# Optimization experiments

Measured on AMD Instinct MI355X. Metric: run time of the kernel, lower is better.

## Reference

```python
import jax, jax.numpy as jnp
import numpy as np

LN_EPS = 1e-12


def _conv1d(x, w, b, pad):
    # x: (B, Cin, L), w: (Cout, Cin, K) -> (B, Cout, L)
    y = jax.lax.conv_general_dilated(x, w, window_strides=(1,), padding=[(pad, pad)],
                                     dimension_numbers=('NCH', 'OIH', 'NCH'))
    return y + b[None, :, None]


def setup_inputs() -> dict:
    key = jax.random.key(0)
    ks = jax.random.split(key, 6)
    B, L, C, KH = 4, 4096, 768, 7
    return {
        'hidden_states': jax.random.normal(ks[0], (B, L, C), jnp.float32),
        'attention_mask': jnp.ones((B, L), jnp.float32),
        'special_tokens_mask': jnp.zeros((B, L), jnp.float32),
        'ln_w': jnp.ones((C,), jnp.float32),
        'ln_b': jnp.zeros((C,), jnp.float32),
        'off_w': jax.random.normal(ks[1], (KH, C, KH), jnp.float32) * 0.02,
        'off_b': jnp.zeros((KH,), jnp.float32),
        'mod_w': jax.random.normal(ks[2], (KH, C, KH), jnp.float32) * 0.02,
        'mod_b': jnp.zeros((KH,), jnp.float32),
        'reg_w': jax.random.normal(ks[3], (C, C, KH), jnp.float32) * 0.02,
    }


def reference(hidden_states, attention_mask, special_tokens_mask,
              ln_w, ln_b, off_w, off_b, mod_w, mod_b, reg_w):
    B, L, C = hidden_states.shape
    kh = off_w.shape[0]
    pad = kh // 2
    residual = hidden_states

    # input layernorm (biased variance, like torch.nn.LayerNorm)
    mu = hidden_states.mean(-1, keepdims=True)
    var = hidden_states.var(-1, keepdims=True)
    h = (hidden_states - mu) * jax.lax.rsqrt(var + LN_EPS) * ln_w + ln_b

    ht = jnp.swapaxes(h, 1, 2)  # (B, C, L)
    off = _conv1d(ht, off_w, off_b, pad)                    # (B, kh, L) seq-axis offsets
    mod = 2.0 * jax.nn.sigmoid(_conv1d(ht, mod_w, mod_b, pad))  # (B, kh, L)

    # mask special tokens / padding before sampling
    gate = ((1.0 - special_tokens_mask) * attention_mask)[:, None, :]
    xm = ht * gate  # (B, C, L)

    # deformable 1D sampling positions: p - pad + k + off[b,k,p]
    base = (jnp.arange(L, dtype=jnp.float32) - pad)[None, :] + jnp.arange(kh, dtype=jnp.float32)[:, None]  # (kh, L)
    pos = base[None, :, :] + off  # (B, kh, L)
    f = jnp.floor(pos)
    t = pos - f                   # (B, kh, L) frac
    fi = f.astype(jnp.int32)

    def gather(idx):
        # linear-sample tap with zero padding outside [0, L-1]
        inb = ((idx >= 0) & (idx <= L - 1)).astype(xm.dtype)  # (B, kh, L)
        idxc = jnp.clip(idx, 0, L - 1)
        v = jax.vmap(lambda xb, ib: xb[:, ib])(xm, idxc)      # (B, C, kh, L)
        return v * inb[:, None, :, :]

    sample = gather(fi) * (1.0 - t)[:, None] + gather(fi + 1) * t[:, None]  # (B, C, kh, L)
    sample = sample * mod[:, None]  # modulated

    out = jnp.einsum('ock,bckp->bop', reg_w, sample)  # (B, C, L)
    out = jnp.swapaxes(out, 1, 2) + residual          # (B, L, C)
    return out
```

## Files before the change

kernel.cpp:

```cpp
#include <hip/hip_runtime.h>
#include <math.h>

#define BB 4
#define LL 4096
#define CC 768
#define KHH 7
#define PADK 3
#define ROWS (BB*LL)
#define NKP  (BB*KHH*LL)
#define GK   (KHH*CC)
#define NT   (GK/64)
#define NKC  (GK/8)

typedef unsigned short ushort8 __attribute__((ext_vector_type(8)));
typedef unsigned short ushort4v __attribute__((ext_vector_type(4)));
typedef short short8 __attribute__((ext_vector_type(8)));
typedef float f32x4 __attribute__((ext_vector_type(4)));
typedef unsigned int uint4v __attribute__((ext_vector_type(4)));

__device__ __forceinline__ float bf2f(unsigned short u) {
    return __uint_as_float(((unsigned)u) << 16);
}
__device__ __forceinline__ unsigned short f2bf(float x) {
    unsigned u = __float_as_uint(x);
    return (unsigned short)((u + 0x7FFFu + ((u >> 16) & 1u)) >> 16);
}
__device__ __forceinline__ unsigned cvtpk(float lo, float hi) {
    unsigned r;
    asm("v_cvt_pk_bf16_f32 %0, %1, %2" : "=v"(r) : "v"(lo), "v"(hi));
    return r;
}

__global__ __launch_bounds__(64) void k_ln(const float* __restrict__ x,
        const float* __restrict__ mask, const float* __restrict__ special,
        const float* __restrict__ lnw, const float* __restrict__ lnb,
        unsigned short* __restrict__ hb, float* __restrict__ gate) {
    int row = blockIdx.x;
    int t = threadIdx.x;
    const float4* xr = (const float4*)(x + (size_t)row * CC);
    float4 v0 = xr[t], v1 = xr[t + 64], v2 = xr[t + 128];
    float s = v0.x + v0.y + v0.z + v0.w
            + v1.x + v1.y + v1.z + v1.w
            + v2.x + v2.y + v2.z + v2.w;
    float q = v0.x * v0.x + v0.y * v0.y + v0.z * v0.z + v0.w * v0.w
            + v1.x * v1.x + v1.y * v1.y + v1.z * v1.z + v1.w * v1.w
            + v2.x * v2.x + v2.y * v2.y + v2.z * v2.z + v2.w * v2.w;
    for (int o = 32; o; o >>= 1) { s += __shfl_xor(s, o); q += __shfl_xor(q, o); }
    float mu  = s * (1.f / CC);
    float var = fmaxf(q * (1.f / CC) - mu * mu, 0.f);
    float rstd = rsqrtf(var + 1e-12f);
    const float4* lw = (const float4*)lnw;
    const float4* lb = (const float4*)lnb;
    ushort4v* hr = (ushort4v*)(hb + (size_t)row * CC);
#pragma unroll
    for (int j = 0; j < 3; ++j) {
        int i4 = t + 64 * j;
        float4 v = (j == 0) ? v0 : (j == 1) ? v1 : v2;
        float4 w = lw[i4], bso = lb[i4];
        ushort4v r;
        r[0] = f2bf((v.x - mu) * rstd * w.x + bso.x);
        r[1] = f2bf((v.y - mu) * rstd * w.y + bso.y);
        r[2] = f2bf((v.z - mu) * rstd * w.z + bso.z);
        r[3] = f2bf((v.w - mu) * rstd * w.w + bso.w);
        hr[i4] = r;
    }
    if (t == 0) gate[row] = (1.f - special[row]) * mask[row];
}

__global__ __launch_bounds__(256) void k_wbt(const float* __restrict__ rw,
                                             unsigned short* __restrict__ wbt) {
    __shared__ float s[4 * GK];
    int o0 = blockIdx.x * 4;
    for (int i = threadIdx.x; i < 4 * GK; i += 256)
        s[i] = rw[(size_t)(o0 + i / GK) * GK + (i % GK)];
    __syncthreads();
    for (int kc = threadIdx.x; kc < NKC; kc += 256) {
        int k = kc / 96;
        int c0 = (kc - k * 96) * 8;
        unsigned short* dst = wbt + ((size_t)kc * CC + o0) * 8;
#pragma unroll
        for (int oo = 0; oo < 4; ++oo) {
            ushort8 r;
#pragma unroll
            for (int e = 0; e < 8; ++e) r[e] = f2bf(s[oo * GK + (c0 + e) * KHH + k]);
            *(ushort8*)(dst + oo * 8) = r;
        }
    }
}

__global__ __launch_bounds__(256) void k_wcb(const float* __restrict__ ow, const float* __restrict__ mw,
                                             unsigned short* __restrict__ wcb) {
    int i = blockIdx.x;
    for (int c = threadIdx.x; c < CC; c += 256) {
        float v = 0.f;
        if (i < 49)      v = ow[(size_t)(i / 7) * (CC * KHH) + (size_t)c * KHH + (i % 7)];
        else if (i < 98) { int j = i - 49; v = mw[(size_t)(j / 7) * (CC * KHH) + (size_t)c * KHH + (j % 7)]; }
        wcb[(size_t)i * CC + c] = f2bf(v);
    }
}

__global__ __launch_bounds__(256) void k_dg2(const unsigned short* __restrict__ A,
        const unsigned short* __restrict__ Bm, float* __restrict__ d) {
    __shared__ __align__(16) char As[64 * 128];
    __shared__ __align__(16) char Bs[128 * 128];
    int r0 = blockIdx.x * 64;
    int t = threadIdx.x;
    int lane = t & 63, w = t >> 6;
    int wr = w >> 1, wc = w & 1;
    f32x4 acc[2][4];
#pragma unroll
    for (int m = 0; m < 2; ++m)
#pragma unroll
        for (int n = 0; n < 4; ++n) acc[m][n] = (f32x4){0.f, 0.f, 0.f, 0.f};
    int lr = lane & 15;
    int lkb0 = (lane >> 4) * 16;
    for (int kk = 0; kk < CC; kk += 64) {
#pragma unroll
        for (int s = 0; s < 2; ++s) {
            int byteoff = (s * 256 + t) * 16;
            int row = byteoff >> 7;
            int colb = byteoff & 127;
            int sw = (row * 128 + colb) ^ ((row & 7) << 4);
            *(ushort8*)(As + sw) = *(const ushort8*)(A + (size_t)(r0 + row) * CC + kk + (colb >> 1));
        }
#pragma unroll
        for (int s = 0; s < 4; ++s) {
            int byteoff = (s * 256 + t) * 16;
            int row = byteoff >> 7;
            int colb = byteoff & 127;
            int sw = (row * 128 + colb) ^ ((row & 7) << 4);
            *(ushort8*)(Bs + sw) = *(const ushort8*)(Bm + (size_t)row * CC + kk + (colb >> 1));
        }
        __syncthreads();
#pragma unroll
        for (int ks = 0; ks < 2; ++ks) {
            short8 av[2], bv[4];
            int lkb = lkb0 + ks * 64;
#pragma unroll
            for (int m = 0; m < 2; ++m) {
                int ar = wr * 32 + m * 16 + lr;
                av[m] = *(const short8*)(As + ((ar * 128 + lkb) ^ ((ar & 7) << 4)));
            }
#pragma unroll
            for (int n = 0; n < 4; ++n) {
                int br = wc * 64 + n * 16 + lr;
                bv[n] = *(const short8*)(Bs + ((br * 128 + lkb) ^ ((br & 7) << 4)));
            }
#pragma unroll
            for (int m = 0; m < 2; ++m)
#pragma unroll
                for (int n = 0; n < 4; ++n)
                    acc[m][n] = __builtin_amdgcn_mfma_f32_16x16x32_bf16(av[m], bv[n], acc[m][n], 0, 0, 0);
        }
        __syncthreads();
    }
    int lr4 = (lane >> 4) * 4, lc = lane & 15;
#pragma unroll
    for (int m = 0; m < 2; ++m) {
        int gr = r0 + wr * 32 + m * 16 + lr4;
#pragma unroll
        for (int n = 0; n < 4; ++n) {
            int gc = wc * 64 + n * 16 + lc;
#pragma unroll
            for (int j = 0; j < 4; ++j)
                d[(size_t)(gr + j) * 128 + gc] = acc[m][n][j];
        }
    }
}

__global__ __launch_bounds__(256) void k_off(const float* __restrict__ d,
        const float* __restrict__ offb, const float* __restrict__ modb,
        const float* __restrict__ gate,
        int* __restrict__ idx0, int* __restrict__ idx1,
        float* __restrict__ w0a, float* __restrict__ w1a) {
    int flat = blockIdx.x * 256 + threadIdx.x;
    if (flat >= NKP) return;
    int p = flat & (LL - 1);
    int k = (flat >> 12) % KHH;
    int b = flat / (KHH * LL);
    float offa = offb[k], moda = modb[k];
#pragma unroll
    for (int j = 0; j < KHH; ++j) {
        int q = p + j - PADK;
        if (q >= 0 && q < LL) {
            const float* dr = d + (size_t)(b * LL + q) * 128;
            offa += dr[k * 7 + j];
            moda += dr[49 + k * 7 + j];
        }
    }
    float modv = 2.f / (1.f + expf(-moda));
    float pos = (float)(p - PADK + k) + offa;
    pos = fminf(fmaxf(pos, -1.0e9f), 1.0e9f);
    float f = floorf(pos);
    float tf = pos - f;
    int i0 = (int)f;
    int i1 = i0 + 1;
    float in0 = (i0 >= 0 && i0 < LL) ? 1.f : 0.f;
    float in1 = (i1 >= 0 && i1 < LL) ? 1.f : 0.f;
    int c0 = min(max(i0, 0), LL - 1);
    int c1 = min(max(i1, 0), LL - 1);
    float g0 = gate[b * LL + c0] * in0;
    float g1 = gate[b * LL + c1] * in1;
    w0a[flat] = modv * (1.f - tf) * g0;
    w1a[flat] = modv * tf * g1;
    idx0[flat] = c0;
    idx1[flat] = c1;
}


#define STEPOFF 49152
#define KSOFF   24576

#define LOADB3(Q, KS, D0, D1, D2) do { \
    const unsigned short* _q = (Q) + (KS) * KSOFF; \
    D0 = *(const short8*)(_q); \
    D1 = *(const short8*)(_q + 128); \
    D2 = *(const short8*)(_q + 256); \
} while (0)

#define MFMA_ROW3(AV, M, B0, B1, B2) \
    acc[M][0] = __builtin_amdgcn_mfma_f32_16x16x32_bf16(AV, B0, acc[M][0], 0, 0, 0); \
    acc[M][1] = __builtin_amdgcn_mfma_f32_16x16x32_bf16(AV, B1, acc[M][1], 0, 0, 0); \
    acc[M][2] = __builtin_amdgcn_mfma_f32_16x16x32_bf16(AV, B2, acc[M][2], 0, 0, 0);

#define COMPUTE_KS3(ASB, KS, B0, B1, B2) do { \
    __builtin_amdgcn_s_setprio(1); \
    int _lkb = ke0 * 2 + (KS) * 64; \
    short8 _av0, _av1, _av2, _av3, _av4, _av5, _av6, _av7; \
    { int ar = 0 * 16 + lr; _av0 = *(const short8*)((ASB) + ar * 128 + (_lkb ^ ((ar & 7) << 4))); } \
    { int ar = 1 * 16 + lr; _av1 = *(const short8*)((ASB) + ar * 128 + (_lkb ^ ((ar & 7) << 4))); } \
    { int ar = 2 * 16 + lr; _av2 = *(const short8*)((ASB) + ar * 128 + (_lkb ^ ((ar & 7) << 4))); } \
    { int ar = 3 * 16 + lr; _av3 = *(const short8*)((ASB) + ar * 128 + (_lkb ^ ((ar & 7) << 4))); } \
    MFMA_ROW3(_av0, 0, B0, B1, B2) \
    MFMA_ROW3(_av1, 1, B0, B1, B2) \
    MFMA_ROW3(_av2, 2, B0, B1, B2) \
    MFMA_ROW3(_av3, 3, B0, B1, B2) \
    { int ar = 4 * 16 + lr; _av4 = *(const short8*)((ASB) + ar * 128 + (_lkb ^ ((ar & 7) << 4))); } \
    { int ar = 5 * 16 + lr; _av5 = *(const short8*)((ASB) + ar * 128 + (_lkb ^ ((ar & 7) << 4))); } \
    { int ar = 6 * 16 + lr; _av6 = *(const short8*)((ASB) + ar * 128 + (_lkb ^ ((ar & 7) << 4))); } \
    { int ar = 7 * 16 + lr; _av7 = *(const short8*)((ASB) + ar * 128 + (_lkb ^ ((ar & 7) << 4))); } \
    MFMA_ROW3(_av4, 4, B0, B1, B2) \
    MFMA_ROW3(_av5, 5, B0, B1, B2) \
    MFMA_ROW3(_av6, 6, B0, B1, B2) \
    MFMA_ROW3(_av7, 7, B0, B1, B2) \
    __builtin_amdgcn_s_setprio(0); \
} while (0)

#define BAR() do { \
    asm volatile("s_waitcnt lgkmcnt(0)" ::: "memory"); \
    __builtin_amdgcn_s_barrier(); \
    __builtin_amdgcn_sched_barrier(0); \
} while (0)

__global__ __launch_bounds__(512, 2) void k_fgemm(const unsigned short* __restrict__ hb,
        const unsigned short* __restrict__ Wbt,
        const int* __restrict__ idx0, const int* __restrict__ idx1,
        const float* __restrict__ w0a, const float* __restrict__ w1a,
        const float* __restrict__ resid, float* __restrict__ out) {
    __shared__ __align__(16) char As[2][128 * 128];

    int bid = blockIdx.x;
    int nhalf = (bid & 7) >> 2;
    int rowtile = (bid >> 3) * 4 + (bid & 3);
    int r0 = rowtile * 128;
    int o0 = nhalf * 384;
    int b = r0 >> 12;
    int p0 = r0 & (LL - 1);
    int pbase = ((b * KHH) << 12) + p0;
    const unsigned short* hbB = hb + (size_t)b * LL * CC;

    int t = threadIdx.x;
    int lane = t & 63, wc = t >> 6;
    int lr = lane & 15;
    int ke0 = (lane >> 4) * 8;

    const unsigned short* pB = Wbt + ((size_t)(lane >> 4) * CC + o0 + wc * 48 + lr) * 8;

    int arow = t >> 2, aseg = t & 3;
    int acolb = aseg * 32;
    int aswz0 = arow * 128 + (acolb ^ ((arow & 7) << 4));
    int aswz1 = arow * 128 + ((acolb + 16) ^ ((arow & 7) << 4));

    f32x4 acc[8][3];
#pragma unroll
    for (int m = 0; m < 8; ++m)
#pragma unroll
        for (int n = 0; n < 3; ++n) acc[m][n] = (f32x4){0.f, 0.f, 0.f, 0.f};

    float wa = 0.f, wbv = 0.f;
    int cur_tap = -1;
    const unsigned short* pA0 = hbB;
    const unsigned short* pA1 = hbB;

    ushort8 la0, la1, la2, la3;
    short8 S0_0, S0_1, S0_2;
    short8 S1_0, S1_1, S1_2;
    short8 S2_0, S2_1, S2_2;

    auto loadA = [&](int tap, int c0) {
        if (tap != cur_tap) {
            int pf = pbase + (tap << 12) + arow;
            int g0 = idx0[pf], g1 = idx1[pf];
            wa = w0a[pf];  wbv = w1a[pf];
            cur_tap = tap;
            pA0 = hbB + (size_t)g0 * CC + c0 + aseg * 16;
            pA1 = hbB + (size_t)g1 * CC + c0 + aseg * 16;
        } else {
            pA0 += 64;
            pA1 += 64;
        }
        la0 = *(const ushort8*)(pA0);
        la1 = *(const ushort8*)(pA0 + 8);
        la2 = *(const ushort8*)(pA1);
        la3 = *(const ushort8*)(pA1 + 8);
    };

    auto writeA = [&](char* Asb) {
        uint4v va, vb;
#pragma unroll
        for (int p = 0; p < 4; ++p) {
            float lo = fmaf(wa, bf2f(la0[2 * p]),     wbv * bf2f(la2[2 * p]));
            float hi = fmaf(wa, bf2f(la0[2 * p + 1]), wbv * bf2f(la2[2 * p + 1]));
            va[p] = cvtpk(lo, hi);
        }
#pragma unroll
        for (int p = 0; p < 4; ++p) {
            float lo = fmaf(wa, bf2f(la1[2 * p]),     wbv * bf2f(la3[2 * p]));
            float hi = fmaf(wa, bf2f(la1[2 * p + 1]), wbv * bf2f(la3[2 * p + 1]));
            vb[p] = cvtpk(lo, hi);
        }
        *(uint4v*)(Asb + aswz0) = va;
        *(uint4v*)(Asb + aswz1) = vb;
    };

    loadA(0, 0);
    LOADB3(pB, 0, S0_0, S0_1, S0_2);
    LOADB3(pB, 1, S1_0, S1_1, S1_2);
    writeA(As[0]);
    BAR();

    int tap_c = 0, c0_c = 0;
    for (int sp = 0; sp < NT; sp += 2) {
        {
            int tap_n = tap_c, c0_n = c0_c + 64;
            if (c0_n == CC) { c0_n = 0; ++tap_n; }
            bool more = (sp + 1 < NT);
            const unsigned short* pN = pB + STEPOFF;
            if (more) {
                LOADB3(pN, 0, S2_0, S2_1, S2_2);
                loadA(tap_n, c0_n);
            }
            __builtin_amdgcn_sched_barrier(0);
            COMPUTE_KS3(As[0], 0, S0_0, S0_1, S0_2);
            COMPUTE_KS3(As[0], 1, S1_0, S1_1, S1_2);
            if (more) {
                LOADB3(pN, 1, S1_0, S1_1, S1_2);
                writeA(As[1]);
            }
            BAR();
            pB = pN;
            tap_c = tap_n; c0_c = c0_n;
        }
        {
            int s = sp + 1;
            if (s >= NT) break;
            int tap_n = tap_c, c0_n = c0_c + 64;
            if (c0_n == CC) { c0_n = 0; ++tap_n; }
            bool more = (s + 1 < NT);
            const unsigned short* pN = pB + STEPOFF;
            if (more) {
                LOADB3(pN, 0, S0_0, S0_1, S0_2);
                loadA(tap_n, c0_n);
            }
            __builtin_amdgcn_sched_barrier(0);
            COMPUTE_KS3(As[1], 0, S2_0, S2_1, S2_2);
            COMPUTE_KS3(As[1], 1, S1_0, S1_1, S1_2);
            if (more) {
                LOADB3(pN, 1, S1_0, S1_1, S1_2);
                writeA(As[0]);
            }
            BAR();
            pB = pN;
            tap_c = tap_n; c0_c = c0_n;
        }
    }

    int lr4 = (lane >> 4) * 4, lc = lane & 15;
#pragma unroll
    for (int m = 0; m < 8; ++m) {
        int gr = r0 + m * 16 + lr4;
#pragma unroll
        for (int n = 0; n < 3; ++n) {
            int gc = o0 + wc * 48 + n * 16 + lc;
#pragma unroll
            for (int j = 0; j < 4; ++j) {
                size_t idx = (size_t)(gr + j) * CC + gc;
                out[idx] = acc[m][n][j] + resid[idx];
            }
        }
    }
}

extern "C" void kernel_launch(void* const* d_in, const int* in_sizes, int n_in,
                              void* d_out, int out_size, void* d_ws, size_t ws_size,
                              hipStream_t stream) {
    const float* x   = (const float*)d_in[0];
    const float* am  = (const float*)d_in[1];
    const float* stm = (const float*)d_in[2];
    const float* lnw = (const float*)d_in[3];
    const float* lnb = (const float*)d_in[4];
    const float* ow  = (const float*)d_in[5];
    const float* ob  = (const float*)d_in[6];
    const float* mw  = (const float*)d_in[7];
    const float* mb  = (const float*)d_in[8];
    const float* rw  = (const float*)d_in[9];
    float* out = (float*)d_out;

    char* ws = (char*)d_ws;
    size_t off = 0;
    auto carve = [&](size_t bytes) -> char* {
        char* p = ws + off;
        off += (bytes + 255) & ~(size_t)255;
        return p;
    };
    unsigned short* hb  = (unsigned short*)carve((size_t)ROWS * CC * 2);
    unsigned short* wbt = (unsigned short*)carve((size_t)NKC * CC * 8 * 2);
    unsigned short* wcb = (unsigned short*)carve((size_t)128 * CC * 2);
    float* d    = (float*)carve((size_t)ROWS * 128 * 4);
    float* gate = (float*)carve((size_t)ROWS * 4);
    int*   i0   = (int*)carve((size_t)NKP * 4);
    int*   i1   = (int*)carve((size_t)NKP * 4);
    float* w0   = (float*)carve((size_t)NKP * 4);
    float* w1   = (float*)carve((size_t)NKP * 4);

    k_ln<<<ROWS, 64, 0, stream>>>(x, am, stm, lnw, lnb, hb, gate);
    k_wbt<<<CC / 4, 256, 0, stream>>>(rw, wbt);
    k_wcb<<<128, 256, 0, stream>>>(ow, mw, wcb);
    k_dg2<<<ROWS / 64, 256, 0, stream>>>(hb, wcb, d);
    k_off<<<NKP / 256, 256, 0, stream>>>(d, ob, mb, gate, i0, i1, w0, w1);
    k_fgemm<<<256, 512, 0, stream>>>(hb, wbt, i0, i1, w0, w1, x, out);
}
```

Baseline: 184.9 us.

## Fuse offset/modulation GEMM with sampling-index kernel using halo rows in LDS

```diff
diff --git a/kernel.cpp b/kernel.cpp
--- a/kernel.cpp
+++ b/kernel.cpp
@@ -99,112 +99,124 @@
     }
 }
 
-__global__ __launch_bounds__(256) void k_dg2(const unsigned short* __restrict__ A,
-        const unsigned short* __restrict__ Bm, float* __restrict__ d) {
-    __shared__ __align__(16) char As[64 * 128];
+__global__ __launch_bounds__(256, 2) void k_dgoff(const unsigned short* __restrict__ hb,
+        const unsigned short* __restrict__ wcb,
+        const float* __restrict__ offb, const float* __restrict__ modb,
+        const float* __restrict__ gate,
+        int* __restrict__ idx0, int* __restrict__ idx1,
+        float* __restrict__ w0a, float* __restrict__ w1a) {
+    __shared__ __align__(16) char As[80 * 128];
     __shared__ __align__(16) char Bs[128 * 128];
+    __shared__ float ds[80][130];
+
     int r0 = blockIdx.x * 64;
+    int b = r0 >> 12;
+    int p0 = r0 & (LL - 1);
+    const unsigned short* hbB = hb + (size_t)b * LL * CC;
+
     int t = threadIdx.x;
-    int lane = t & 63, w = t >> 6;
-    int wr = w >> 1, wc = w & 1;
-    f32x4 acc[2][4];
-#pragma unroll
-    for (int m = 0; m < 2; ++m)
-#pragma unroll
-        for (int n = 0; n < 4; ++n) acc[m][n] = (f32x4){0.f, 0.f, 0.f, 0.f};
+    int lane = t & 63, wc = t >> 6;
     int lr = lane & 15;
     int lkb0 = (lane >> 4) * 16;
+
+    f32x4 acc[5][2];
+#pragma unroll
+    for (int m = 0; m < 5; ++m)
+#pragma unroll
+        for (int n = 0; n < 2; ++n) acc[m][n] = (f32x4){0.f, 0.f, 0.f, 0.f};
+
     for (int kk = 0; kk < CC; kk += 64) {
 #pragma unroll
-        for (int s = 0; s < 2; ++s) {
+        for (int s = 0; s < 3; ++s) {
             int byteoff = (s * 256 + t) * 16;
-            int row = byteoff >> 7;
-            int colb = byteoff & 127;
-            int sw = (row * 128 + colb) ^ ((row & 7) << 4);
-            *(ushort8*)(As + sw) = *(const ushort8*)(A + (size_t)(r0 + row) * CC + kk + (colb >> 1));
+            if (byteoff < 80 * 128) {
+                int row = byteoff >> 7;
+                int colb = byteoff & 127;
+                int pl = p0 - 8 + row;
+                ushort8 v;
+#pragma unroll
+                for (int e = 0; e < 8; ++e) v[e] = 0;
+                if (pl >= 0 && pl < LL)
+                    v = *(const ushort8*)(hbB + (size_t)pl * CC + kk + (colb >> 1));
+                *(ushort8*)(As + row * 128 + (colb ^ ((row & 7) << 4))) = v;
+            }
         }
 #pragma unroll
         for (int s = 0; s < 4; ++s) {
             int byteoff = (s * 256 + t) * 16;
             int row = byteoff >> 7;
             int colb = byteoff & 127;
-            int sw = (row * 128 + colb) ^ ((row & 7) << 4);
-            *(ushort8*)(Bs + sw) = *(const ushort8*)(Bm + (size_t)row * CC + kk + (colb >> 1));
+            *(ushort8*)(Bs + row * 128 + (colb ^ ((row & 7) << 4))) =
+                *(const ushort8*)(wcb + (size_t)row * CC + kk + (colb >> 1));
         }
         __syncthreads();
 #pragma unroll
         for (int ks = 0; ks < 2; ++ks) {
-            short8 av[2], bv[4];
+            short8 av[5], bv[2];
             int lkb = lkb0 + ks * 64;
 #pragma unroll
-            for (int m = 0; m < 2; ++m) {
-                int ar = wr * 32 + m * 16 + lr;
-                av[m] = *(const short8*)(As + ((ar * 128 + lkb) ^ ((ar & 7) << 4)));
-            }
-#pragma unroll
-            for (int n = 0; n < 4; ++n) {
-                int br = wc * 64 + n * 16 + lr;
-                bv[n] = *(const short8*)(Bs + ((br * 128 + lkb) ^ ((br & 7) << 4)));
-            }
-#pragma unroll
-            for (int m = 0; m < 2; ++m)
-#pragma unroll
-                for (int n = 0; n < 4; ++n)
+            for (int m = 0; m < 5; ++m) {
+                int ar = m * 16 + lr;
+                av[m] = *(const short8*)(As + ar * 128 + (lkb ^ ((ar & 7) << 4)));
+            }
+#pragma unroll
+            for (int n = 0; n < 2; ++n) {
+                int br = wc * 32 + n * 16 + lr;
+                bv[n] = *(const short8*)(Bs + br * 128 + (lkb ^ ((br & 7) << 4)));
+            }
+#pragma unroll
+            for (int m = 0; m < 5; ++m)
+#pragma unroll
+                for (int n = 0; n < 2; ++n)
                     acc[m][n] = __builtin_amdgcn_mfma_f32_16x16x32_bf16(av[m], bv[n], acc[m][n], 0, 0, 0);
         }
         __syncthreads();
     }
     int lr4 = (lane >> 4) * 4, lc = lane & 15;
 #pragma unroll
-    for (int m = 0; m < 2; ++m) {
-        int gr = r0 + wr * 32 + m * 16 + lr4;
-#pragma unroll
-        for (int n = 0; n < 4; ++n) {
-            int gc = wc * 64 + n * 16 + lc;
+    for (int m = 0; m < 5; ++m) {
+#pragma unroll
+        for (int n = 0; n < 2; ++n) {
+            int gc = wc * 32 + n * 16 + lc;
 #pragma unroll
             for (int j = 0; j < 4; ++j)
-                d[(size_t)(gr + j) * 128 + gc] = acc[m][n][j];
-        }
-    }
-}
-
-__global__ __launch_bounds__(256) void k_off(const float* __restrict__ d,
-        const float* __restrict__ offb, const float* __restrict__ modb,
-        const float* __restrict__ gate,
-        int* __restrict__ idx0, int* __restrict__ idx1,
-        float* __restrict__ w0a, float* __restrict__ w1a) {
-    int flat = blockIdx.x * 256 + threadIdx.x;
-    if (flat >= NKP) return;
-    int p = flat & (LL - 1);
-    int k = (flat >> 12) % KHH;
-    int b = flat / (KHH * LL);
-    float offa = offb[k], moda = modb[k];
-#pragma unroll
-    for (int j = 0; j < KHH; ++j) {
-        int q = p + j - PADK;
-        if (q >= 0 && q < LL) {
-            const float* dr = d + (size_t)(b * LL + q) * 128;
-            offa += dr[k * 7 + j];
-            moda += dr[49 + k * 7 + j];
-        }
-    }
-    float modv = 2.f / (1.f + expf(-moda));
-    float pos = (float)(p - PADK + k) + offa;
-    pos = fminf(fmaxf(pos, -1.0e9f), 1.0e9f);
-    float f = floorf(pos);
-    float tf = pos - f;
-    int i0 = (int)f;
-    int i1 = i0 + 1;
-    float in0 = (i0 >= 0 && i0 < LL) ? 1.f : 0.f;
-    float in1 = (i1 >= 0 && i1 < LL) ? 1.f : 0.f;
-    int c0 = min(max(i0, 0), LL - 1);
-    int c1 = min(max(i1, 0), LL - 1);
-    float g0 = gate[b * LL + c0] * in0;
-    float g1 = gate[b * LL + c1] * in1;
-    w0a[flat] = modv * (1.f - tf) * g0;
-    w1a[flat] = modv * tf * g1;
-    idx0[flat] = c0;
-    idx1[flat] = c1;
+                ds[m * 16 + lr4 + j][gc] = acc[m][n][j];
+        }
+    }
+    __syncthreads();
+
+    for (int it = t; it < 64 * KHH; it += 256) {
+        int pl = it / KHH;
+        int k  = it - pl * KHH;
+        int p  = p0 + pl;
+        float offa = offb[k], moda = modb[k];
+#pragma unroll
+        for (int j = 0; j < KHH; ++j) {
+            int qg = p + j - PADK;
+            if (qg >= 0 && qg < LL) {
+                offa += ds[pl + j + 5][k * 7 + j];
+                moda += ds[pl + j + 5][49 + k * 7 + j];
+            }
+        }
+        float modv = 2.f / (1.f + expf(-moda));
+        float pos = (float)(p - PADK + k) + offa;
+        pos = fminf(fmaxf(pos, -1.0e9f), 1.0e9f);
+        float f = floorf(pos);
+        float tf = pos - f;
+        int i0 = (int)f;
+        int i1 = i0 + 1;
+        float in0 = (i0 >= 0 && i0 < LL) ? 1.f : 0.f;
+        float in1 = (i1 >= 0 && i1 < LL) ? 1.f : 0.f;
+        int c0 = min(max(i0, 0), LL - 1);
+        int c1 = min(max(i1, 0), LL - 1);
+        float g0 = gate[b * LL + c0] * in0;
+        float g1 = gate[b * LL + c1] * in1;
+        int flat = ((b * KHH + k) << 12) + p;
+        w0a[flat] = modv * (1.f - tf) * g0;
+        w1a[flat] = modv * tf * g1;
+        idx0[flat] = c0;
+        idx1[flat] = c1;
+    }
 }
 
 
@@ -426,7 +438,6 @@
     unsigned short* hb  = (unsigned short*)carve((size_t)ROWS * CC * 2);
     unsigned short* wbt = (unsigned short*)carve((size_t)NKC * CC * 8 * 2);
     unsigned short* wcb = (unsigned short*)carve((size_t)128 * CC * 2);
-    float* d    = (float*)carve((size_t)ROWS * 128 * 4);
     float* gate = (float*)carve((size_t)ROWS * 4);
     int*   i0   = (int*)carve((size_t)NKP * 4);
     int*   i1   = (int*)carve((size_t)NKP * 4);
@@ -436,7 +447,6 @@
     k_ln<<<ROWS, 64, 0, stream>>>(x, am, stm, lnw, lnb, hb, gate);
     k_wbt<<<CC / 4, 256, 0, stream>>>(rw, wbt);
     k_wcb<<<128, 256, 0, stream>>>(ow, mw, wcb);
-    k_dg2<<<ROWS / 64, 256, 0, stream>>>(hb, wcb, d);
-    k_off<<<NKP / 256, 256, 0, stream>>>(d, ob, mb, gate, i0, i1, w0, w1);
+    k_dgoff<<<ROWS / 64, 256, 0, stream>>>(hb, wcb, ob, mb, gate, i0, i1, w0, w1);
     k_fgemm<<<256, 512, 0, stream>>>(hb, wbt, i0, i1, w0, w1, x, out);
 }
```

New measurement: 187.5 us. Within noise of the previous version (+1.4%).
